# Optimization experiments

Measured on AMD Instinct MI355X. Metric: run time of the kernel, lower is better.

## Reference

```python
import jax, jax.numpy as jnp
import numpy as np

B = 512
ND, ED = 40, 160
N0, C1, C2 = 706, 512, 400
E0 = 8000
DIM_C = 16
BN_EPS = 1e-5


def _np_graphs():
    rng = np.random.default_rng(0)
    off_d = np.arange(B)[:, None] * ND
    dei = np.stack([(rng.integers(0, ND, (B, ED)) + off_d).ravel(),
                    (rng.integers(0, ND, (B, ED)) + off_d).ravel()]).astype(np.int32)
    dbatch = np.repeat(np.arange(B), ND).astype(np.int32)
    off_c = np.arange(B)[:, None] * N0
    ei0 = np.stack([(rng.integers(0, N0, (B, E0)) + off_c).ravel(),
                    (rng.integers(0, N0, (B, E0)) + off_c).ravel()])

    def surj(n, c):
        a = np.concatenate([np.arange(c), rng.integers(0, c, n - c)])
        rng.shuffle(a)
        return a
    c0, c1 = surj(N0, C1), surj(C1, C2)
    cl0 = (c0[None] + np.arange(B)[:, None] * C1).ravel()
    cl1 = (c1[None] + np.arange(B)[:, None] * C2).ravel()
    # pooled edge_index for GAT layer 1 (PyG max_pool: map, drop self loops, coalesce)
    e1 = cl0[ei0]
    e1 = e1[:, e1[0] != e1[1]]
    e1 = np.unique(e1, axis=1)
    return dei, dbatch, ei0.astype(np.int32), e1.astype(np.int32), cl0.astype(np.int32), cl1.astype(np.int32)


def _bn(x, gamma=None, beta=None):
    # training-mode BatchNorm1d forward (biased batch var), affine optional
    mu = x.mean(0)
    var = x.var(0)
    xh = (x - mu) * jax.lax.rsqrt(var + BN_EPS)
    if gamma is None:
        return xh
    return xh * gamma + beta


def _gat(x, ei, W, a_src, a_dst, bias):
    # PyG GATConv, heads=1, self loops added, leaky_relu slope 0.2
    n = x.shape[0]
    loop = jnp.arange(n, dtype=ei.dtype)
    src = jnp.concatenate([ei[0], loop])
    dst = jnp.concatenate([ei[1], loop])
    h = x @ W  # [N, F]
    logit = jax.nn.leaky_relu((h * a_src).sum(-1)[src] + (h * a_dst).sum(-1)[dst], 0.2)
    m = jax.ops.segment_max(logit, dst, num_segments=n)
    e = jnp.exp(logit - m[dst])
    s = jax.ops.segment_sum(e, dst, num_segments=n)
    alpha = e / s[dst]
    return jax.ops.segment_sum(h[src] * alpha[:, None], dst, num_segments=n) + bias


def _forward(drug_x, cell_x, gin0_W1, gin0_b1, gin0_W2, gin0_b2, gin0_g, gin0_be, gin1_W1, gin1_b1, gin1_W2, gin1_b2, gin1_g, gin1_be, gin2_W1, gin2_b1, gin2_W2, gin2_b2, gin2_g, gin2_be, demb_W, demb_b, gat0_W, gat0_as, gat0_ad, gat0_b, gat1_W, gat1_as, gat1_ad, gat1_b, cemb_W1, cemb_b1, cemb_W2, cemb_b2, reg_W1, reg_b1, reg_W2, reg_b2, reg_W3, reg_b3, drug_edge_index, drug_batch, cell_edge_index0, cell_edge_index1, cluster0, cluster1):
    nd = drug_x.shape[0]
    x = drug_x
    reps = []
    gin = ((gin0_W1, gin0_b1, gin0_W2, gin0_b2, gin0_g, gin0_be),
           (gin1_W1, gin1_b1, gin1_W2, gin1_b2, gin1_g, gin1_be),
           (gin2_W1, gin2_b1, gin2_W2, gin2_b2, gin2_g, gin2_be))
    for W1, b1, W2, b2, g, be in gin:
        agg = jax.ops.segment_sum(x[drug_edge_index[0]], drug_edge_index[1], num_segments=nd)
        x = jax.nn.relu(jax.nn.relu((x + agg) @ W1 + b1) @ W2 + b2)
        x = _bn(x, g, be)
        reps.append(x)
    xd = jax.ops.segment_max(jnp.concatenate(reps, -1), drug_batch, num_segments=B)  # [B,384]
    xd = jax.nn.relu(xd @ demb_W + demb_b)  # dropout = identity (eval)
    # cell branch: GAT + relu, cluster max_pool, BN (affine=False), twice
    xc = jax.nn.relu(_gat(cell_x, cell_edge_index0, gat0_W, gat0_as, gat0_ad, gat0_b))
    xc = _bn(jax.ops.segment_max(xc, cluster0, num_segments=B * C1))
    xc = jax.nn.relu(_gat(xc, cell_edge_index1, gat1_W, gat1_as, gat1_ad, gat1_b))
    xc = _bn(jax.ops.segment_max(xc, cluster1, num_segments=B * C2))
    xc = xc.reshape(B, C2 * DIM_C)
    xc = jax.nn.relu(xc @ cemb_W1 + cemb_b1)
    xc = jax.nn.relu(xc @ cemb_W2 + cemb_b2)
    h = jnp.concatenate([xd, xc], -1)  # [B,384]
    h = jax.nn.elu(h @ reg_W1 + reg_b1)
    h = jax.nn.elu(h @ reg_W2 + reg_b2)
    return h @ reg_W3 + reg_b3  # [B,1]


def setup_inputs():
    dei, dbatch, ei0, ei1, cl0, cl1 = _np_graphs()
    keys = iter(jax.random.split(jax.random.key(0), 64))

    def W(*shape):
        return jax.random.normal(next(keys), shape, jnp.float32) / np.float32(np.sqrt(shape[0]))

    def vec(n):
        return jax.random.normal(next(keys), (n,), jnp.float32) * np.float32(0.3)
    z = lambda n: jnp.zeros((n,), jnp.float32)
    inp = {'drug_x': jax.random.normal(next(keys), (B * ND, 77), jnp.float32),
           'cell_x': jax.random.normal(next(keys), (B * N0, 3), jnp.float32)}
    for i, fin in enumerate((77, 128, 128)):
        inp['gin%d_W1' % i] = W(fin, 128); inp['gin%d_b1' % i] = z(128)
        inp['gin%d_W2' % i] = W(128, 128); inp['gin%d_b2' % i] = z(128)
        inp['gin%d_g' % i] = jnp.ones((128,), jnp.float32); inp['gin%d_be' % i] = z(128)
    inp['demb_W'] = W(3 * 128, 128); inp['demb_b'] = z(128)
    for i, fin in enumerate((3, DIM_C)):
        inp['gat%d_W' % i] = W(fin, DIM_C)
        inp['gat%d_as' % i] = vec(DIM_C)
        inp['gat%d_ad' % i] = vec(DIM_C)
        inp['gat%d_b' % i] = z(DIM_C)
    inp['cemb_W1'] = W(C2 * DIM_C, 1024); inp['cemb_b1'] = z(1024)
    inp['cemb_W2'] = W(1024, 256); inp['cemb_b2'] = z(256)
    inp['reg_W1'] = W(384, 384); inp['reg_b1'] = z(384)
    inp['reg_W2'] = W(384, 384); inp['reg_b2'] = z(384)
    inp['reg_W3'] = W(384, 1); inp['reg_b3'] = z(1)
    inp['drug_edge_index'] = jnp.asarray(dei)
    inp['drug_batch'] = jnp.asarray(dbatch)
    inp['cell_edge_index0'] = jnp.asarray(ei0)
    inp['cell_edge_index1'] = jnp.asarray(ei1)
    inp['cluster0'] = jnp.asarray(cl0)
    inp['cluster1'] = jnp.asarray(cl1)
    return inp


def reference(drug_x, cell_x, gin0_W1, gin0_b1, gin0_W2, gin0_b2, gin0_g, gin0_be, gin1_W1, gin1_b1, gin1_W2, gin1_b2, gin1_g, gin1_be, gin2_W1, gin2_b1, gin2_W2, gin2_b2, gin2_g, gin2_be, demb_W, demb_b, gat0_W, gat0_as, gat0_ad, gat0_b, gat1_W, gat1_as, gat1_ad, gat1_b, cemb_W1, cemb_b1, cemb_W2, cemb_b2, reg_W1, reg_b1, reg_W2, reg_b2, reg_W3, reg_b3, drug_edge_index, drug_batch, cell_edge_index0, cell_edge_index1, cluster0, cluster1):
    return _forward(drug_x, cell_x, gin0_W1, gin0_b1, gin0_W2, gin0_b2, gin0_g, gin0_be, gin1_W1, gin1_b1, gin1_W2, gin1_b2, gin1_g, gin1_be, gin2_W1, gin2_b1, gin2_W2, gin2_b2, gin2_g, gin2_be, demb_W, demb_b, gat0_W, gat0_as, gat0_ad, gat0_b, gat1_W, gat1_as, gat1_ad, gat1_b, cemb_W1, cemb_b1, cemb_W2, cemb_b2, reg_W1, reg_b1, reg_W2, reg_b2, reg_W3, reg_b3, drug_edge_index, drug_batch, cell_edge_index0, cell_edge_index1, cluster0, cluster1)
```

## Files before the change

kernel.cpp:

```cpp
#include <hip/hip_runtime.h>
#include <math.h>

typedef __attribute__((ext_vector_type(8))) short bfrag;
typedef __attribute__((ext_vector_type(4))) float ffrag;

__device__ __forceinline__ unsigned short f2b(float v) {
  return (unsigned short)((__float_as_uint(v) + 0x8000u) >> 16);
}
__device__ __forceinline__ float b2f(unsigned short u) {
  return __uint_as_float((unsigned int)u << 16);
}

__global__ __launch_bounds__(256)
void k_w2bt6(const float* __restrict__ w0, const float* __restrict__ w1,
             const float* __restrict__ w2, const float* __restrict__ w3,
             const float* __restrict__ w4, const float* __restrict__ w5,
             unsigned short* __restrict__ out) {
  int t = blockIdx.x*256 + threadIdx.x;
  if (t >= 128*136) return;
  int L = blockIdx.y;
  const float* W; int Ksrc = 128;
  switch (L) {
    case 0: W = w0; Ksrc = 77; break;
    case 1: W = w1; break;
    case 2: W = w2; break;
    case 3: W = w3; break;
    case 4: W = w4; break;
    default: W = w5; break;
  }
  int n = t / 136, k = t - n*136;
  float v = (k < Ksrc) ? W[(size_t)k*128 + n] : 0.f;
  out[(size_t)L*128*136 + t] = f2b(v);
}

template<int KIN, int BNIN>
__global__ __launch_bounds__(256)
void k_gin_agg_b(const float* __restrict__ xg, const float* __restrict__ st,
                 const int* __restrict__ esrc, const int* __restrict__ edst,
                 unsigned short* __restrict__ xin) {
  __shared__ float xb[40*128];
  __shared__ unsigned short scsr[160];
  __shared__ int srow[41];
  const int b = blockIdx.x, tid = threadIdx.x, nbase = b*40;
  if (tid <= 40) srow[tid] = 0;
  __syncthreads();
  int rs = -1, rd = -1;
  if (tid < 160) {
    rs = esrc[b*160+tid] - nbase;
    rd = edst[b*160+tid] - nbase;
    atomicAdd(&srow[rd+1], 1);
  }
  for (int i = tid; i < 40*KIN; i += 256) {
    int n = i/KIN, f = i - n*KIN;
    float v = xg[(size_t)(nbase+n)*KIN + f];
    if (BNIN) v = fmaf(v, st[f], st[KIN+f]);
    xb[n*128 + f] = v;
  }
  __syncthreads();
  if (tid == 0) { int run = 0; for (int i = 1; i <= 40; ++i) { run += srow[i]; srow[i] = run; } }
  __syncthreads();
  if (tid < 160) { int slot = atomicAdd(&srow[rd], 1); scsr[slot] = (unsigned short)rs; }
  __syncthreads();
  for (int i = tid; i < 40*128; i += 256) {
    int n = i >> 7, f = i & 127;
    float a = 0.f;
    if (f < KIN) {
      a = xb[n*128 + f];
      int j0 = n ? srow[n-1] : 0, j1 = srow[n];
      for (int j = j0; j < j1; ++j) a += xb[scsr[j]*128 + f];
    }
    xin[(size_t)nbase*128 + i] = f2b(a);
  }
}

__global__ __launch_bounds__(512)
void k_gin_fmfma(const unsigned short* __restrict__ Ax,
                 const unsigned short* __restrict__ W1t,
                 const unsigned short* __restrict__ W2t,
                 const float* __restrict__ b1, const float* __restrict__ b2,
                 float* __restrict__ outp, float* __restrict__ bnp) {
  __shared__ unsigned short Ab[128*136];
  __shared__ unsigned short W1l[128*136];
  __shared__ unsigned short W2l[128*136];
  __shared__ float cred[8*128], cred2[8*128];
  const int tid = threadIdx.x;
  const int row0 = blockIdx.x << 7;
  for (int i = tid; i < 128*17; i += 512) {
    int r = i / 17, c8 = (i - r*17) << 3;
    uint4 v = make_uint4(0,0,0,0);
    if (c8 < 128) v = *(const uint4*)(Ax + (size_t)(row0 + r)*128 + c8);
    *(uint4*)&Ab[r*136 + c8]  = v;
    *(uint4*)&W1l[r*136 + c8] = *(const uint4*)(W1t + r*136 + c8);
    *(uint4*)&W2l[r*136 + c8] = *(const uint4*)(W2t + r*136 + c8);
  }
  __syncthreads();
  const int wave = tid >> 6, lane = tid & 63;
  const int fr = lane & 15, fk = (lane >> 4) << 3;
  const int wrow = wave << 4;
  const int mrow = (lane >> 4) << 2;
  float b1v[8], b2v[8];
#pragma unroll
  for (int n = 0; n < 8; ++n) { b1v[n] = b1[(n<<4) + fr]; b2v[n] = b2[(n<<4) + fr]; }

  ffrag acc[8];
#pragma unroll
  for (int n = 0; n < 8; ++n) acc[n] = (ffrag){0.f,0.f,0.f,0.f};
#pragma unroll
  for (int s = 0; s < 4; ++s) {
    bfrag af = *(const bfrag*)&Ab[(wrow + fr)*136 + (s<<5) + fk];
#pragma unroll
    for (int n = 0; n < 8; ++n) {
      bfrag bf = *(const bfrag*)&W1l[((n<<4) + fr)*136 + (s<<5) + fk];
      acc[n] = __builtin_amdgcn_mfma_f32_16x16x32_bf16(af, bf, acc[n], 0, 0, 0);
    }
  }
#pragma unroll
  for (int n = 0; n < 8; ++n)
#pragma unroll
    for (int r = 0; r < 4; ++r) {
      float v = fmaxf(acc[n][r] + b1v[n], 0.f);
      Ab[(wrow + mrow + r)*136 + (n<<4) + fr] = f2b(v);
    }
  __syncthreads();

  ffrag acc2[8];
#pragma unroll
  for (int n = 0; n < 8; ++n) acc2[n] = (ffrag){0.f,0.f,0.f,0.f};
#pragma unroll
  for (int s = 0; s < 4; ++s) {
    bfrag af = *(const bfrag*)&Ab[(wrow + fr)*136 + (s<<5) + fk];
#pragma unroll
    for (int n = 0; n < 8; ++n) {
      bfrag bf = *(const bfrag*)&W2l[((n<<4) + fr)*136 + (s<<5) + fk];
      acc2[n] = __builtin_amdgcn_mfma_f32_16x16x32_bf16(af, bf, acc2[n], 0, 0, 0);
    }
  }
#pragma unroll
  for (int n = 0; n < 8; ++n) {
    float s = 0.f, q = 0.f;
#pragma unroll
    for (int r = 0; r < 4; ++r) {
      float v = fmaxf(acc2[n][r] + b2v[n], 0.f);
      outp[(size_t)(row0 + wrow + mrow + r)*128 + (n<<4) + fr] = v;
      s += v; q = fmaf(v, v, q);
    }
    s += __shfl_xor(s, 16); s += __shfl_xor(s, 32);
    q += __shfl_xor(q, 16); q += __shfl_xor(q, 32);
    if (lane < 16) { cred[wave*128 + (n<<4) + fr] = s; cred2[wave*128 + (n<<4) + fr] = q; }
  }
  __syncthreads();
  if (tid < 128) {
    float S = 0.f, Q = 0.f;
#pragma unroll
    for (int w = 0; w < 8; ++w) { S += cred[w*128 + tid]; Q += cred2[w*128 + tid]; }
    bnp[blockIdx.x*256 + tid] = S;
    bnp[blockIdx.x*256 + 128 + tid] = Q;
  }
}

__global__ __launch_bounds__(128)
void k_drug_pool_bn(const float* __restrict__ p0, const float* __restrict__ p1,
                    const float* __restrict__ p2,
                    const float* __restrict__ s0, const float* __restrict__ s1,
                    const float* __restrict__ s2,
                    float* __restrict__ xd) {
  int b = blockIdx.x, f = threadIdx.x;
  const float* ps[3] = {p0,p1,p2};
  const float* ss[3] = {s0,s1,s2};
#pragma unroll
  for (int L = 0; L < 3; ++L) {
    float sc = ss[L][f], sh = ss[L][128+f];
    float m = -3.0e38f;
    const float* p = ps[L] + (size_t)b*40*128 + f;
    for (int n = 0; n < 40; ++n) m = fmaxf(m, fmaf(p[n*128], sc, sh));
    xd[(size_t)b*384 + L*128 + f] = m;
  }
}

template<int ACT, int PART, int BNA, int NPA, int ACTA, int BNP>
__global__ __launch_bounds__(256)
void k_gemm(const float* __restrict__ A, int lda,
            const float* __restrict__ B, int ldb,
            const float* __restrict__ bias,
            float* __restrict__ C, int ldc, int Kchunk,
            long pstrideC, long pstrideA,
            const float* __restrict__ abias,
            const float* __restrict__ bnst,
            float* __restrict__ bnp) {
  __shared__ __align__(16) float As[32][68];
  __shared__ __align__(16) float Bs[32][68];
  const int tid = threadIdx.x;
  const int tx = tid & 15, ty = tid >> 4;
  const int row0 = blockIdx.y << 6, col0 = blockIdx.x << 6;
  const int kb = blockIdx.z * Kchunk;
  if (PART) C += (size_t)blockIdx.z * pstrideC;
  float acc[4][4] = {{0.f}};
  for (int k0 = 0; k0 < Kchunk; k0 += 32) {
#pragma unroll
    for (int i = 0; i < 2; ++i) {
      int idx = tid + (i << 8);
      int r = idx >> 3, c = (idx & 7) << 2;
      const float* ap = A + (size_t)(row0 + r)*lda + (kb + k0 + c);
      float4 v = *(const float4*)ap;
      if (NPA > 1) {
#pragma unroll
        for (int z = 1; z < NPA; ++z) {
          float4 p = *(const float4*)(ap + (size_t)z*pstrideA);
          v.x += p.x; v.y += p.y; v.z += p.z; v.w += p.w;
        }
        const float* ab = abias + (kb + k0 + c);
        v.x += ab[0]; v.y += ab[1]; v.z += ab[2]; v.w += ab[3];
        if (ACTA == 1) {
          v.x=fmaxf(v.x,0.f); v.y=fmaxf(v.y,0.f); v.z=fmaxf(v.z,0.f); v.w=fmaxf(v.w,0.f);
        } else if (ACTA == 2) {
          v.x = v.x>0.f?v.x:expm1f(v.x); v.y = v.y>0.f?v.y:expm1f(v.y);
          v.z = v.z>0.f?v.z:expm1f(v.z); v.w = v.w>0.f?v.w:expm1f(v.w);
        }
      }
      if (BNA) {
        int fb = (kb + k0 + c) & 15;
        float4 sc = *(const float4*)&bnst[fb];
        float4 sh = *(const float4*)&bnst[16 + fb];
        v.x = fmaf(v.x, sc.x, sh.x); v.y = fmaf(v.y, sc.y, sh.y);
        v.z = fmaf(v.z, sc.z, sh.z); v.w = fmaf(v.w, sc.w, sh.w);
      }
      int sw = ((c >> 2) & 7) << 2;
      int rs = r ^ sw;
      As[c+0][rs]=v.x; As[c+1][rs]=v.y; As[c+2][rs]=v.z; As[c+3][rs]=v.w;
    }
#pragma unroll
    for (int i = 0; i < 2; ++i) {
      int idx = tid + (i << 8);
      int r = idx >> 4, c = (idx & 15) << 2;
      *(float4*)&Bs[r][c] = *(const float4*)(B + (size_t)(kb + k0 + r)*ldb + (col0 + c));
    }
    __syncthreads();
#pragma unroll
    for (int kk = 0; kk < 32; ++kk) {
      int sw = ((kk >> 2) & 7) << 2;
      float4 av = *(const float4*)&As[kk][(ty << 2) ^ sw];
      float4 bv = *(const float4*)&Bs[kk][tx << 2];
      acc[0][0]=fmaf(av.x,bv.x,acc[0][0]); acc[0][1]=fmaf(av.x,bv.y,acc[0][1]);
      acc[0][2]=fmaf(av.x,bv.z,acc[0][2]); acc[0][3]=fmaf(av.x,bv.w,acc[0][3]);
      acc[1][0]=fmaf(av.y,bv.x,acc[1][0]); acc[1][1]=fmaf(av.y,bv.y,acc[1][1]);
      acc[1][2]=fmaf(av.y,bv.z,acc[1][2]); acc[1][3]=fmaf(av.y,bv.w,acc[1][3]);
      acc[2][0]=fmaf(av.z,bv.x,acc[2][0]); acc[2][1]=fmaf(av.z,bv.y,acc[2][1]);
      acc[2][2]=fmaf(av.z,bv.z,acc[2][2]); acc[2][3]=fmaf(av.z,bv.w,acc[2][3]);
      acc[3][0]=fmaf(av.w,bv.x,acc[3][0]); acc[3][1]=fmaf(av.w,bv.y,acc[3][1]);
      acc[3][2]=fmaf(av.w,bv.z,acc[3][2]); acc[3][3]=fmaf(av.w,bv.w,acc[3][3]);
    }
    __syncthreads();
  }
#pragma unroll
  for (int i = 0; i < 4; ++i) {
    int r = row0 + (ty<<2) + i, c = col0 + (tx<<2);
    float4 v = make_float4(acc[i][0], acc[i][1], acc[i][2], acc[i][3]);
    if (!PART) {
      if (bias) { v.x += bias[c]; v.y += bias[c+1]; v.z += bias[c+2]; v.w += bias[c+3]; }
      if (ACT == 1) { v.x=fmaxf(v.x,0.f); v.y=fmaxf(v.y,0.f); v.z=fmaxf(v.z,0.f); v.w=fmaxf(v.w,0.f); }
      else if (ACT == 2) {
        v.x = v.x>0.f?v.x:expm1f(v.x); v.y = v.y>0.f?v.y:expm1f(v.y);
        v.z = v.z>0.f?v.z:expm1f(v.z); v.w = v.w>0.f?v.w:expm1f(v.w);
      }
    }
    *(float4*)(C + (size_t)r*ldc + c) = v;
  }
}

template<int ACT>
__global__ void k_reduce(const float* __restrict__ parts, int np, long pstride,
                         const float* __restrict__ bias,
                         float* __restrict__ out, int ldo, int M, int N) {
  int t = blockIdx.x*blockDim.x + threadIdx.x;
  if (t >= M*N) return;
  int r = t / N, c = t - r*N;
  float s = 0.f;
  for (int z = 0; z < np; ++z) s += parts[(size_t)z*pstride + t];
  s += bias[c];
  if (ACT == 1) s = fmaxf(s, 0.f);
  else if (ACT == 2) s = s > 0.f ? s : expm1f(s);
  out[(size_t)r*ldo + c] = s;
}

__global__ __launch_bounds__(256)
void k_w2bt(const float* __restrict__ W, unsigned short* __restrict__ Bt) {
  __shared__ float tile[32][33];
  int bk = blockIdx.x << 5, bn = blockIdx.y << 5;
  int c = threadIdx.x & 31, r8 = threadIdx.x >> 5;
#pragma unroll
  for (int i = 0; i < 4; ++i) {
    int r = r8 + (i << 3);
    tile[r][c] = W[(size_t)(bk + r)*1024 + bn + c];
  }
  __syncthreads();
#pragma unroll
  for (int i = 0; i < 4; ++i) {
    int r = r8 + (i << 3);
    Bt[(size_t)(bn + r)*6400 + bk + c] = f2b(tile[c][r]);
  }
}

__global__ void k_a2bn(const float* __restrict__ x, const float* __restrict__ st,
                       unsigned short* __restrict__ o, int total4) {
  int t = blockIdx.x*blockDim.x + threadIdx.x;
  if (t >= total4) return;
  int fb = (t << 2) & 15;
  float4 v = *(const float4*)(x + ((size_t)t << 2));
  float4 sc = *(const float4*)&st[fb];
  float4 sh = *(const float4*)&st[16 + fb];
  ushort4 r;
  r.x = f2b(fmaf(v.x, sc.x, sh.x));
  r.y = f2b(fmaf(v.y, sc.y, sh.y));
  r.z = f2b(fmaf(v.z, sc.z, sh.z));
  r.w = f2b(fmaf(v.w, sc.w, sh.w));
  *(ushort4*)(o + ((size_t)t << 2)) = r;
}

__global__ __launch_bounds__(256)
void k_mfma128(const unsigned short* __restrict__ A,
               const unsigned short* __restrict__ Bt,
               float* __restrict__ C, int ldc, int K,
               int Kchunk, long pstrideC) {
  __shared__ unsigned short Al[2][128*40];
  __shared__ unsigned short Bl[2][128*40];
  const int tid = threadIdx.x;
  const int row0 = blockIdx.y << 7, col0 = blockIdx.x << 7;
  const int kb = blockIdx.z * Kchunk;
  C += (size_t)blockIdx.z * pstrideC;
  const int wave = tid >> 6, lane = tid & 63;
  const int wr = wave >> 1, wc = wave & 1;
  const int fr = lane & 15, fk = (lane >> 4) << 3;
  const int lr = tid >> 1, lco = (tid & 1) << 4;

  ffrag acc[4][4];
#pragma unroll
  for (int i = 0; i < 4; ++i)
#pragma unroll
    for (int n = 0; n < 4; ++n) acc[i][n] = (ffrag){0.f, 0.f, 0.f, 0.f};

  const unsigned short* ag = A  + (size_t)(row0 + lr)*K + kb + lco;
  const unsigned short* bg = Bt + (size_t)(col0 + lr)*K + kb + lco;

  uint4 ra0 = *(const uint4*)ag, ra1 = *(const uint4*)(ag + 8);
  uint4 rb0 = *(const uint4*)bg, rb1 = *(const uint4*)(bg + 8);
  *(uint4*)&Al[0][lr*40 + lco] = ra0; *(uint4*)&Al[0][lr*40 + lco + 8] = ra1;
  *(uint4*)&Bl[0][lr*40 + lco] = rb0; *(uint4*)&Bl[0][lr*40 + lco + 8] = rb1;
  __syncthreads();

  const int NS = Kchunk >> 5;
  int cur = 0;
  for (int s = 0; s < NS; ++s) {
    if (s + 1 < NS) {
      const unsigned short* an = ag + ((s + 1) << 5);
      const unsigned short* bn = bg + ((s + 1) << 5);
      ra0 = *(const uint4*)an; ra1 = *(const uint4*)(an + 8);
      rb0 = *(const uint4*)bn; rb1 = *(const uint4*)(bn + 8);
    }
    bfrag af[4], bf[4];
#pragma unroll
    for (int i = 0; i < 4; ++i) af[i] = *(const bfrag*)&Al[cur][(wr*64 + i*16 + fr)*40 + fk];
#pragma unroll
    for (int n = 0; n < 4; ++n) bf[n] = *(const bfrag*)&Bl[cur][(wc*64 + n*16 + fr)*40 + fk];
#pragma unroll
    for (int i = 0; i < 4; ++i)
#pragma unroll
      for (int n = 0; n < 4; ++n)
        acc[i][n] = __builtin_amdgcn_mfma_f32_16x16x32_bf16(af[i], bf[n], acc[i][n], 0, 0, 0);
    if (s + 1 < NS) {
      cur ^= 1;
      *(uint4*)&Al[cur][lr*40 + lco] = ra0; *(uint4*)&Al[cur][lr*40 + lco + 8] = ra1;
      *(uint4*)&Bl[cur][lr*40 + lco] = rb0; *(uint4*)&Bl[cur][lr*40 + lco + 8] = rb1;
      __syncthreads();
    }
  }
  const int frow = (lane >> 4) << 2;
#pragma unroll
  for (int i = 0; i < 4; ++i)
#pragma unroll
    for (int n = 0; n < 4; ++n) {
      float* cp = C + (size_t)(row0 + wr*64 + i*16 + frow)*ldc + col0 + wc*64 + n*16 + fr;
#pragma unroll
      for (int r = 0; r < 4; ++r) cp[(size_t)r*ldc] = acc[i][n][r];
    }
}

__global__ void k_bn_fin(const float* __restrict__ parts, int nb, int C, float invn,
                         const float* __restrict__ g, const float* __restrict__ be,
                         float* __restrict__ stats) {
  int f = threadIdx.x;
  if (f >= C) return;
  float s = 0.f, s2 = 0.f;
#pragma unroll 4
  for (int z = 0; z < nb; ++z) { s += parts[z*2*C + f]; s2 += parts[z*2*C + C + f]; }
  float mu = s*invn;
  float var = fmaxf(s2*invn - mu*mu, 0.f);
  float rstd = rsqrtf(var + 1e-5f);
  float sc = g ? g[f]*rstd : rstd;
  stats[f] = sc;
  stats[C+f] = (be ? be[f] : 0.f) - mu*sc;
}

template<int NODES, int NPOOL, int KIN, int MAXE, int SORTED, int BNIN, int NT>
__global__ __launch_bounds__(NT, 8)
void k_gat_lds(const float* __restrict__ x,
               const int* __restrict__ esrc, const int* __restrict__ edst, int Earg,
               const float* __restrict__ W, const float* __restrict__ as_,
               const float* __restrict__ ad_, const float* __restrict__ bias,
               const int* __restrict__ cluster,
               const float* __restrict__ instats,
               float* __restrict__ pooled, float* __restrict__ bnp) {
  constexpr int EIT = (MAXE + NT - 1) / NT;
  __shared__ unsigned int shp[NODES*9];
  __shared__ unsigned int spk[MAXE];
  __shared__ float sss[NODES], ssd[NODES];
  __shared__ int srow[NODES+1];
  __shared__ float sWl[KIN*16 + 16];
  __shared__ float sas[16], sad[16];
  __shared__ int schunk[32];
  __shared__ int sr2[2];
  const int b = blockIdx.x;
  const int tid = threadIdx.x;
  const int nbase = b*NODES;

  if (tid < KIN*16) sWl[tid] = W[tid];
  if (tid >= 64 && tid < 80)  sWl[KIN*16 + tid-64] = bias[tid-64];
  if (tid >= 80 && tid < 96)  sas[tid-80] = as_[tid-80];
  if (tid >= 96 && tid < 112) sad[tid-96] = ad_[tid-96];
  if (SORTED && tid == 0) {
    int a = 0, c = Earg;
    while (a < c) { int m = (a+c) >> 1; if (esrc[m] < nbase) a = m+1; else c = m; }
    sr2[0] = a;
    c = Earg;
    int nend = nbase + NODES;
    while (a < c) { int m = (a+c) >> 1; if (esrc[m] < nend) a = m+1; else c = m; }
    sr2[1] = a;
  }
  for (int i = tid; i <= NODES; i += NT) srow[i] = 0;
  __syncthreads();

  int e0, Eblk;
  if (SORTED) { e0 = sr2[0]; Eblk = sr2[1] - sr2[0]; }
  else        { e0 = b*Earg; Eblk = Earg; }

  int ers[EIT], erd[EIT];
#pragma unroll
  for (int it = 0; it < EIT; ++it) {
    int e = tid + it*NT;
    ers[it] = -1; erd[it] = -1;
    if (e < Eblk) {
      ers[it] = esrc[e0+e] - nbase;
      erd[it] = edst[e0+e] - nbase;
      atomicAdd(&srow[erd[it]+1], 1);
    }
  }
  for (int i = tid; i < NODES*16; i += NT) {
    int n = i >> 4, f = i & 15;
    const float* xp = x + (size_t)(nbase + n)*KIN;
    float xq = (f < KIN) ? xp[f] : 0.f;
    if (BNIN && f < KIN) xq = fmaf(xq, instats[f], instats[16+f]);
    float hv = 0.f;
#pragma unroll
    for (int j = 0; j < KIN; ++j) hv = fmaf(__shfl(xq, j, 16), sWl[j*16 + f], hv);
    unsigned int hb = (unsigned int)f2b(hv);
    unsigned int partner = (unsigned int)__shfl_xor((int)hb, 1);
    if ((f & 1) == 0) shp[n*9 + (f >> 1)] = hb | (partner << 16);
    float s1 = hv * sas[f], s2 = hv * sad[f];
#pragma unroll
    for (int m = 8; m >= 1; m >>= 1) { s1 += __shfl_xor(s1, m); s2 += __shfl_xor(s2, m); }
    if (f == 0) { sss[n] = s1; ssd[n] = s2; }
  }
  __syncthreads();

  constexpr int NC = 32, CS = (NODES + NC - 1) / NC;
  if (tid < NC) {
    int run = 0, lo = tid*CS, hi = (tid+1)*CS < NODES ? (tid+1)*CS : NODES;
    for (int i = lo; i < hi; ++i) { run += srow[i+1]; srow[i+1] = run; }
    schunk[tid] = run;
  }
  __syncthreads();
  if (tid == 0) { int base = 0; for (int c = 0; c < NC; ++c) { int t2 = schunk[c]; schunk[c] = base; base += t2; } }
  __syncthreads();
  for (int i = tid; i < NODES; i += NT) srow[i+1] += schunk[i/CS];
  __syncthreads();

#pragma unroll
  for (int it = 0; it < EIT; ++it) {
    if (erd[it] >= 0) {
      int slot = atomicAdd(&srow[erd[it]], 1);
      float l = sss[ers[it]] + ssd[erd[it]];
      l = fmaxf(l, 0.2f*l);
      float ex = __expf(l);
      spk[slot] = ((__float_as_uint(ex) + 0x8000u) & 0xffff0000u) | (unsigned int)ers[it];
    }
  }
  __syncthreads();

  {
    const int lane = tid & 7, grp = tid >> 3;
    for (int n = grp; n < NODES; n += (NT >> 3)) {
      float ls = sss[n] + ssd[n];
      ls = fmaxf(ls, 0.2f*ls);
      float exs = __expf(ls);
      unsigned int hp = shp[n*9 + lane];
      float aLo = exs * b2f((unsigned short)hp);
      float aHi = exs * b2f((unsigned short)(hp >> 16));
      float sum = exs;
      int j = (n > 0) ? srow[n-1] : 0, j1 = srow[n];
      for (; j + 4 <= j1; j += 4) {
        unsigned int p0 = spk[j], p1 = spk[j+1], p2 = spk[j+2], p3 = spk[j+3];
        float e0 = __uint_as_float(p0 & 0xffff0000u);
        float e1 = __uint_as_float(p1 & 0xffff0000u);
        float e2 = __uint_as_float(p2 & 0xffff0000u);
        float e3 = __uint_as_float(p3 & 0xffff0000u);
        unsigned int h0 = shp[(p0 & 0xffffu)*9 + lane];
        unsigned int h1 = shp[(p1 & 0xffffu)*9 + lane];
        unsigned int h2 = shp[(p2 & 0xffffu)*9 + lane];
        unsigned int h3 = shp[(p3 & 0xffffu)*9 + lane];
        aLo = fmaf(e0, b2f((unsigned short)h0), aLo);
        aHi = fmaf(e0, b2f((unsigned short)(h0 >> 16)), aHi); sum += e0;
        aLo = fmaf(e1, b2f((unsigned short)h1), aLo);
        aHi = fmaf(e1, b2f((unsigned short)(h1 >> 16)), aHi); sum += e1;
        aLo = fmaf(e2, b2f((unsigned short)h2), aLo);
        aHi = fmaf(e2, b2f((unsigned short)(h2 >> 16)), aHi); sum += e2;
        aLo = fmaf(e3, b2f((unsigned short)h3), aLo);
        aHi = fmaf(e3, b2f((unsigned short)(h3 >> 16)), aHi); sum += e3;
      }
      for (; j < j1; ++j) {
        unsigned int p0 = spk[j];
        float e0 = __uint_as_float(p0 & 0xffff0000u);
        unsigned int h0 = shp[(p0 & 0xffffu)*9 + lane];
        aLo = fmaf(e0, b2f((unsigned short)h0), aLo);
        aHi = fmaf(e0, b2f((unsigned short)(h0 >> 16)), aHi); sum += e0;
      }
      float inv = 1.f / sum;
      float vLo = fmaxf(fmaf(aLo, inv, sWl[KIN*16 + 2*lane]), 0.f);
      float vHi = fmaxf(fmaf(aHi, inv, sWl[KIN*16 + 2*lane + 1]), 0.f);
      int* pp = (int*)pooled + (size_t)cluster[nbase + n]*16 + 2*lane;
      atomicMax(pp,     __float_as_int(vLo));
      atomicMax(pp + 1, __float_as_int(vHi));
    }
  }
  __syncthreads();

  {
    float s = 0.f, q = 0.f;
    const float* po = pooled + (size_t)b*NPOOL*16;
    int f = tid & 15;
    for (int r = tid >> 4; r < NPOOL; r += (NT >> 4)) {
      float v = po[r*16 + f];
      s += v; q = fmaf(v, v, q);
    }
    float* red = (float*)shp;
    red[tid] = s; red[NT + tid] = q;
    __syncthreads();
    for (int o = NT >> 1; o >= 16; o >>= 1) {
      if (tid < o) { red[tid] += red[tid + o]; red[NT + tid] += red[NT + tid + o]; }
      __syncthreads();
    }
    if (tid < 16) { bnp[b*32 + tid] = red[tid]; bnp[b*32 + 16 + tid] = red[NT + tid]; }
  }
}

__global__ __launch_bounds__(64)
void k_gemv_out(const float* __restrict__ parts, long pstrideA,
                const float* __restrict__ abias,
                const float* __restrict__ w,
                const float* __restrict__ b, float* __restrict__ out) {
  int r = blockIdx.x, l = threadIdx.x;
  float s = 0.f;
  for (int k = l; k < 384; k += 64) {
    const float* p = parts + (size_t)r*384 + k;
    float h = p[0] + p[pstrideA] + p[2*pstrideA] + p[3*pstrideA] + abias[k];
    h = h > 0.f ? h : expm1f(h);
    s = fmaf(h, w[k], s);
  }
#pragma unroll
  for (int o = 32; o > 0; o >>= 1) s += __shfl_down(s, o);
  if (l == 0) out[r] = s + b[0];
}

extern "C" void kernel_launch(void* const* d_in, const int* in_sizes, int n_in,
                              void* d_out, int out_size, void* d_ws, size_t ws_size,
                              hipStream_t stream) {
  (void)n_in; (void)out_size;
  const int B = 512;
  const int nd  = B*40;
  const int nc1 = B*512;
  const int nc2 = B*400;
  const int Ec0 = in_sizes[42]/2;
  const int Ec1 = in_sizes[43]/2;

  const float* drug_x = (const float*)d_in[0];
  const float* cell_x = (const float*)d_in[1];
  const float* gW1[3] = {(const float*)d_in[2],(const float*)d_in[8],(const float*)d_in[14]};
  const float* gb1[3] = {(const float*)d_in[3],(const float*)d_in[9],(const float*)d_in[15]};
  const float* gW2[3] = {(const float*)d_in[4],(const float*)d_in[10],(const float*)d_in[16]};
  const float* gb2[3] = {(const float*)d_in[5],(const float*)d_in[11],(const float*)d_in[17]};
  const float* gg [3] = {(const float*)d_in[6],(const float*)d_in[12],(const float*)d_in[18]};
  const float* gbe[3] = {(const float*)d_in[7],(const float*)d_in[13],(const float*)d_in[19]};
  const float* demb_W = (const float*)d_in[20]; const float* demb_b = (const float*)d_in[21];
  const float* gatW[2]  = {(const float*)d_in[22],(const float*)d_in[26]};
  const float* gatAS[2] = {(const float*)d_in[23],(const float*)d_in[27]};
  const float* gatAD[2] = {(const float*)d_in[24],(const float*)d_in[28]};
  const float* gatB[2]  = {(const float*)d_in[25],(const float*)d_in[29]};
  const float* cembW1 = (const float*)d_in[30]; const float* cembb1 = (const float*)d_in[31];
  const float* cembW2 = (const float*)d_in[32]; const float* cembb2 = (const float*)d_in[33];
  const float* regW1 = (const float*)d_in[34]; const float* regb1 = (const float*)d_in[35];
  const float* regW2 = (const float*)d_in[36]; const float* regb2 = (const float*)d_in[37];
  const float* regW3 = (const float*)d_in[38]; const float* regb3 = (const float*)d_in[39];
  const int* dei = (const int*)d_in[40];
  const int* ei0 = (const int*)d_in[42];
  const int* ei1 = (const int*)d_in[43];
  const int* cl0 = (const int*)d_in[44];
  const int* cl1 = (const int*)d_in[45];
  const int Ed  = in_sizes[40]/2;
  const int *dsrc = dei, *ddst = dei + Ed;
  const int *src0 = ei0, *dst0 = ei0 + Ec0;
  const int *src1 = ei1, *dst1 = ei1 + Ec1;
  float* out = (float*)d_out;

  char* base = (char*)d_ws; size_t off = 0;
  auto AL = [&](size_t bytes)->char* { char* p = base + off; off = (off + bytes + 255) & ~(size_t)255; return p; };
  float* h_cat   = (float*)AL((size_t)512*384*4);
  float* xd      = (float*)AL((size_t)512*384*4);
  float* pooled1 = (float*)AL((size_t)nc1*16*4);
  float* pooled2 = (float*)AL((size_t)nc2*16*4);
  float* st_g0   = (float*)AL(256*4);
  float* st_g1   = (float*)AL(256*4);
  float* st_g2   = (float*)AL(256*4);
  float* st16_0  = (float*)AL(32*4);
  float* st16_1  = (float*)AL(32*4);
  float* bparts  = (float*)AL((size_t)512*256*4);
  unsigned short* Wt6 = (unsigned short*)AL((size_t)6*128*136*2);
  char*  S       = base + off;
  if (ws_size < off + (size_t)53*1024*1024) return;

  dim3 b256(256);

  float* pre0 = (float*)(S);
  float* pre1 = pre0 + (size_t)nd*128;
  float* pre2 = pre1 + (size_t)nd*128;
  unsigned short* xin_b = (unsigned short*)(pre2 + (size_t)nd*128);
  float* pre[3] = {pre0, pre1, pre2};
  float* stg[3] = {st_g0, st_g1, st_g2};

  size_t so = 0;
  auto SB = [&](size_t bytes)->char* { char* p = S + so; so = (so + bytes + 255) & ~(size_t)255; return p; };
  unsigned short* Abf = (unsigned short*)SB((size_t)512*6400*2);
  unsigned short* Btb = (unsigned short*)SB((size_t)1024*6400*2);
  float* parts1 = (float*)SB((size_t)8*512*1024*4);
  float* parts2 = (float*)SB((size_t)8*512*256*4);
  float* partsA = (float*)SB((size_t)4*512*384*4);
  float* partsB = (float*)SB((size_t)4*512*384*4);
  float* cembh = (float*)Abf;

  k_w2bt6<<<dim3(68, 6), b256, 0, stream>>>(gW1[0], gW1[1], gW1[2],
                                            gW2[0], gW2[1], gW2[2], Wt6);
  for (int L = 0; L < 3; ++L) {
    if (L == 0)
      k_gin_agg_b<77,0><<<dim3(512), b256, 0, stream>>>(drug_x, nullptr, dsrc, ddst, xin_b);
    else
      k_gin_agg_b<128,1><<<dim3(512), b256, 0, stream>>>(pre[L-1], stg[L-1], dsrc, ddst, xin_b);
    k_gin_fmfma<<<dim3(160), dim3(512), 0, stream>>>(
        xin_b, Wt6 + (size_t)L*128*136, Wt6 + (size_t)(3+L)*128*136,
        gb1[L], gb2[L], pre[L], bparts);
    k_bn_fin<<<dim3(1), dim3(128), 0, stream>>>(bparts, 160, 128, 1.f/nd, gg[L], gbe[L], stg[L]);
  }
  k_drug_pool_bn<<<dim3(512), dim3(128), 0, stream>>>(pre0, pre1, pre2, st_g0, st_g1, st_g2, xd);
  k_gemm<1,0,0,0,0,0><<<dim3(2,8,1), b256, 0, stream>>>(
      xd, 384, demb_W, 128, demb_b, h_cat, 384, 384, 0, 0, nullptr, nullptr, nullptr);

  k_w2bt<<<dim3(200, 32), b256, 0, stream>>>(cembW1, Btb);

  k_gat_lds<706,512,3,8000,0,0,1024><<<dim3(512), dim3(1024), 0, stream>>>(
      cell_x, src0, dst0, Ec0/512, gatW[0], gatAS[0], gatAD[0], gatB[0], cl0,
      nullptr, pooled1, bparts);
  k_bn_fin<<<dim3(1), dim3(16), 0, stream>>>(bparts, 512, 16, 1.f/nc1, nullptr, nullptr, st16_0);

  k_gat_lds<512,400,16,8000,1,1,1024><<<dim3(512), dim3(1024), 0, stream>>>(
      pooled1, src1, dst1, Ec1, gatW[1], gatAS[1], gatAD[1], gatB[1], cl1,
      st16_0, pooled2, bparts);
  k_bn_fin<<<dim3(1), dim3(16), 0, stream>>>(bparts, 512, 16, 1.f/nc2, nullptr, nullptr, st16_1);

  k_a2bn<<<dim3(3200), b256, 0, stream>>>(pooled2, st16_1, Abf, 512*6400/4);
  k_mfma128<<<dim3(8, 4, 8), b256, 0, stream>>>(
      Abf, Btb, parts1, 1024, 6400, 800, (long)512*1024);
  k_reduce<1><<<dim3((512*1024+255)/256), b256, 0, stream>>>(
      parts1, 8, (long)512*1024, cembb1, cembh, 1024, 512, 1024);
  k_gemm<0,1,0,0,0,0><<<dim3(4,8,8), b256, 0, stream>>>(
      cembh, 1024, cembW2, 256, nullptr, parts2, 256, 128,
      (long)512*256, 0, nullptr, nullptr, nullptr);
  k_reduce<1><<<dim3((512*256+255)/256), b256, 0, stream>>>(
      parts2, 8, (long)512*256, cembb2, h_cat + 128, 384, 512, 256);

  k_gemm<0,1,0,0,0,0><<<dim3(6,8,4), b256, 0, stream>>>(
      h_cat, 384, regW1, 384, nullptr, partsA, 384, 96,
      (long)512*384, 0, nullptr, nullptr, nullptr);
  k_gemm<0,1,0,4,2,0><<<dim3(6,8,4), b256, 0, stream>>>(
      partsA, 384, regW2, 384, nullptr, partsB, 384, 96,
      (long)512*384, (long)512*384, regb1, nullptr, nullptr);
  k_gemv_out<<<dim3(512), dim3(64), 0, stream>>>(
      partsB, (long)512*384, regb2, regW3, regb3, out);
}
```

Baseline: 429.1 us.

## Shrink GIN MLP tiles to 64 rows, read weights from global; parallelize BN finalize

The fused GIN MLP kernel now processes 64 rows per 256-thread block (320 blocks instead of 160) and no longer stages the two weight matrices in LDS. The weight fragments are loaded straight from global memory and rely on cache reuse. This cuts LDS use per block so more blocks fit per CU and more CUs are busy. The BatchNorm finalize kernel now uses 512 threads that split the partial-sum reduction across chunks with a shared-memory tree, replacing single-thread-per-feature serial loops over 160-512 partials. The risk is extra global and L2 traffic for the repeated weight fragment loads.

```diff
diff --git a/kernel.cpp b/kernel.cpp
--- a/kernel.cpp
+++ b/kernel.cpp
@@ -73,25 +73,21 @@
   }
 }
 
-__global__ __launch_bounds__(512)
+__global__ __launch_bounds__(256)
 void k_gin_fmfma(const unsigned short* __restrict__ Ax,
                  const unsigned short* __restrict__ W1t,
                  const unsigned short* __restrict__ W2t,
                  const float* __restrict__ b1, const float* __restrict__ b2,
                  float* __restrict__ outp, float* __restrict__ bnp) {
-  __shared__ unsigned short Ab[128*136];
-  __shared__ unsigned short W1l[128*136];
-  __shared__ unsigned short W2l[128*136];
-  __shared__ float cred[8*128], cred2[8*128];
+  __shared__ unsigned short Ab[64*136];
+  __shared__ float cred[4*128], cred2[4*128];
   const int tid = threadIdx.x;
-  const int row0 = blockIdx.x << 7;
-  for (int i = tid; i < 128*17; i += 512) {
+  const int row0 = blockIdx.x << 6;
+  for (int i = tid; i < 64*17; i += 256) {
     int r = i / 17, c8 = (i - r*17) << 3;
     uint4 v = make_uint4(0,0,0,0);
     if (c8 < 128) v = *(const uint4*)(Ax + (size_t)(row0 + r)*128 + c8);
-    *(uint4*)&Ab[r*136 + c8]  = v;
-    *(uint4*)&W1l[r*136 + c8] = *(const uint4*)(W1t + r*136 + c8);
-    *(uint4*)&W2l[r*136 + c8] = *(const uint4*)(W2t + r*136 + c8);
+    *(uint4*)&Ab[r*136 + c8] = v;
   }
   __syncthreads();
   const int wave = tid >> 6, lane = tid & 63;
@@ -110,7 +106,7 @@
     bfrag af = *(const bfrag*)&Ab[(wrow + fr)*136 + (s<<5) + fk];
 #pragma unroll
     for (int n = 0; n < 8; ++n) {
-      bfrag bf = *(const bfrag*)&W1l[((n<<4) + fr)*136 + (s<<5) + fk];
+      bfrag bf = *(const bfrag*)&W1t[((n<<4) + fr)*136 + (s<<5) + fk];
       acc[n] = __builtin_amdgcn_mfma_f32_16x16x32_bf16(af, bf, acc[n], 0, 0, 0);
     }
   }
@@ -131,7 +127,7 @@
     bfrag af = *(const bfrag*)&Ab[(wrow + fr)*136 + (s<<5) + fk];
 #pragma unroll
     for (int n = 0; n < 8; ++n) {
-      bfrag bf = *(const bfrag*)&W2l[((n<<4) + fr)*136 + (s<<5) + fk];
+      bfrag bf = *(const bfrag*)&W2t[((n<<4) + fr)*136 + (s<<5) + fk];
       acc2[n] = __builtin_amdgcn_mfma_f32_16x16x32_bf16(af, bf, acc2[n], 0, 0, 0);
     }
   }
@@ -152,7 +148,7 @@
   if (tid < 128) {
     float S = 0.f, Q = 0.f;
 #pragma unroll
-    for (int w = 0; w < 8; ++w) { S += cred[w*128 + tid]; Q += cred2[w*128 + tid]; }
+    for (int w = 0; w < 4; ++w) { S += cred[w*128 + tid]; Q += cred2[w*128 + tid]; }
     bnp[blockIdx.x*256 + tid] = S;
     bnp[blockIdx.x*256 + 128 + tid] = Q;
   }
@@ -384,20 +380,34 @@
     }
 }
 
-__global__ void k_bn_fin(const float* __restrict__ parts, int nb, int C, float invn,
-                         const float* __restrict__ g, const float* __restrict__ be,
-                         float* __restrict__ stats) {
-  int f = threadIdx.x;
-  if (f >= C) return;
-  float s = 0.f, s2 = 0.f;
-#pragma unroll 4
-  for (int z = 0; z < nb; ++z) { s += parts[z*2*C + f]; s2 += parts[z*2*C + C + f]; }
-  float mu = s*invn;
-  float var = fmaxf(s2*invn - mu*mu, 0.f);
-  float rstd = rsqrtf(var + 1e-5f);
-  float sc = g ? g[f]*rstd : rstd;
-  stats[f] = sc;
-  stats[C+f] = (be ? be[f] : 0.f) - mu*sc;
+__global__ __launch_bounds__(512)
+void k_bn_fin(const float* __restrict__ parts, int nb, int C, float invn,
+              const float* __restrict__ g, const float* __restrict__ be,
+              float* __restrict__ stats) {
+  __shared__ float rs[512], rq[512];
+  const int tid = threadIdx.x;
+  const int f = tid % C;
+  const int chunks = 512 / C;
+  const int c = tid / C;
+  float s = 0.f, q = 0.f;
+  for (int z = c; z < nb; z += chunks) {
+    s += parts[(size_t)z*2*C + f];
+    q += parts[(size_t)z*2*C + C + f];
+  }
+  rs[tid] = s; rq[tid] = q;
+  __syncthreads();
+  for (int o = 256; o >= C; o >>= 1) {
+    if (tid < o) { rs[tid] += rs[tid + o]; rq[tid] += rq[tid + o]; }
+    __syncthreads();
+  }
+  if (tid < C) {
+    float mu = rs[tid]*invn;
+    float var = fmaxf(rq[tid]*invn - mu*mu, 0.f);
+    float rstd = rsqrtf(var + 1e-5f);
+    float sc = g ? g[tid]*rstd : rstd;
+    stats[tid] = sc;
+    stats[C+tid] = (be ? be[tid] : 0.f) - mu*sc;
+  }
 }
 
 template<int NODES, int NPOOL, int KIN, int MAXE, int SORTED, int BNIN, int NT>
@@ -661,10 +671,10 @@
       k_gin_agg_b<77,0><<<dim3(512), b256, 0, stream>>>(drug_x, nullptr, dsrc, ddst, xin_b);
     else
       k_gin_agg_b<128,1><<<dim3(512), b256, 0, stream>>>(pre[L-1], stg[L-1], dsrc, ddst, xin_b);
-    k_gin_fmfma<<<dim3(160), dim3(512), 0, stream>>>(
+    k_gin_fmfma<<<dim3(320), b256, 0, stream>>>(
         xin_b, Wt6 + (size_t)L*128*136, Wt6 + (size_t)(3+L)*128*136,
         gb1[L], gb2[L], pre[L], bparts);
-    k_bn_fin<<<dim3(1), dim3(128), 0, stream>>>(bparts, 160, 128, 1.f/nd, gg[L], gbe[L], stg[L]);
+    k_bn_fin<<<dim3(1), dim3(512), 0, stream>>>(bparts, 320, 128, 1.f/nd, gg[L], gbe[L], stg[L]);
   }
   k_drug_pool_bn<<<dim3(512), dim3(128), 0, stream>>>(pre0, pre1, pre2, st_g0, st_g1, st_g2, xd);
   k_gemm<1,0,0,0,0,0><<<dim3(2,8,1), b256, 0, stream>>>(
@@ -675,12 +685,12 @@
   k_gat_lds<706,512,3,8000,0,0,1024><<<dim3(512), dim3(1024), 0, stream>>>(
       cell_x, src0, dst0, Ec0/512, gatW[0], gatAS[0], gatAD[0], gatB[0], cl0,
       nullptr, pooled1, bparts);
-  k_bn_fin<<<dim3(1), dim3(16), 0, stream>>>(bparts, 512, 16, 1.f/nc1, nullptr, nullptr, st16_0);
+  k_bn_fin<<<dim3(1), dim3(512), 0, stream>>>(bparts, 512, 16, 1.f/nc1, nullptr, nullptr, st16_0);
 
   k_gat_lds<512,400,16,8000,1,1,1024><<<dim3(512), dim3(1024), 0, stream>>>(
       pooled1, src1, dst1, Ec1, gatW[1], gatAS[1], gatAD[1], gatB[1], cl1,
       st16_0, pooled2, bparts);
-  k_bn_fin<<<dim3(1), dim3(16), 0, stream>>>(bparts, 512, 16, 1.f/nc2, nullptr, nullptr, st16_1);
+  k_bn_fin<<<dim3(1), dim3(512), 0, stream>>>(bparts, 512, 16, 1.f/nc2, nullptr, nullptr, st16_1);
 
   k_a2bn<<<dim3(3200), b256, 0, stream>>>(pooled2, st16_1, Abf, 512*6400/4);
   k_mfma128<<<dim3(8, 4, 8), b256, 0, stream>>>(
```

Result: faster. 399.9 us (-6.8%).
